# Performance work log

Measured on AMD Instinct MI355X. Metric: run time of the kernel, lower is better.

## Reference

```python
import jax, jax.numpy as jnp
import numpy as np

N_NODES = 100000
N_EDGES = 1600000
D = 64


def setup_inputs() -> dict:
    key = jax.random.key(0)
    k0, k1, k2, k3 = jax.random.split(key, 4)
    x = jax.random.normal(k0, (N_NODES, D), dtype=jnp.float32)
    edge_index = jax.random.randint(k1, (2, N_EDGES), 0, N_NODES, dtype=jnp.int64)
    W1 = jax.random.normal(k2, (D, D), dtype=jnp.float32) * 0.1
    b1 = jnp.zeros((D,), dtype=jnp.float32)
    W2 = jax.random.normal(k3, (D, D), dtype=jnp.float32) * 0.1
    b2 = jnp.zeros((D,), dtype=jnp.float32)
    return {"x": x, "edge_index": edge_index, "W1": W1, "b1": b1, "W2": W2, "b2": b2}


def _gcn_layer(x, edge_index, W, b):
    n = x.shape[0]
    h = x @ W  # [N, Dout] -- transform before aggregation (small GEMM)
    loop = jnp.arange(n, dtype=edge_index.dtype)
    src = jnp.concatenate([edge_index[0], loop])
    dst = jnp.concatenate([edge_index[1], loop])
    deg = jax.ops.segment_sum(jnp.ones_like(dst, dtype=h.dtype), dst, num_segments=n)
    dinv = jax.lax.rsqrt(deg)  # deg >= 1 thanks to self loops
    norm = dinv[src] * dinv[dst]  # [E+N]
    msg = h[src] * norm[:, None]  # gather: [E+N, Dout]
    agg = jax.ops.segment_sum(msg, dst, num_segments=n)  # scatter-add
    return agg + b


def reference(x, edge_index, W1, b1, W2, b2):
    # dropout p = 0.0 -> identity
    h = jax.nn.relu(_gcn_layer(x, edge_index, W1, b1))
    h = jax.nn.relu(_gcn_layer(h, edge_index, W2, b2))
    return h
```

## Files before the change

kernel.cpp:

```cpp
#include <hip/hip_runtime.h>
#include <hip/hip_bf16.h>

#define D 64
#define NB_HIST 256
#define MAXBK 512

typedef float vfloat4 __attribute__((ext_vector_type(4)));

__device__ __forceinline__ unsigned short f2bf(float f) {
    union { float f; unsigned u; } v; v.f = f;
    unsigned r = (v.u + 0x7FFF + ((v.u >> 16) & 1)) >> 16;
    return (unsigned short)r;
}
__device__ __forceinline__ float bflo(unsigned u) {
    union { unsigned u; float f; } v; v.u = u << 16; return v.f;
}
__device__ __forceinline__ float bfhi(unsigned u) {
    union { unsigned u; float f; } v; v.u = u & 0xFFFF0000u; return v.f;
}

__global__ __launch_bounds__(256) void passA_gemm(
    const int* __restrict__ dst, int* __restrict__ blockCounts, int E, int per, int NBK,
    const float* __restrict__ X, const float* __restrict__ W,
    unsigned short* __restrict__ hn, int N)
{
    int tid = threadIdx.x;

    if ((int)blockIdx.x < NB_HIST) {
        __shared__ int hist[MAXBK];
        for (int i = tid; i < NBK; i += 256) hist[i] = 0;
        __syncthreads();
        int lo = blockIdx.x * per, hi = min(E, lo + per);
        for (int i = lo + tid * 4; i < hi; i += 1024) {
            if (i + 3 < hi) {
                int4 d4 = *(const int4*)(dst + i);
                atomicAdd(&hist[d4.x >> 8], 1);
                atomicAdd(&hist[d4.y >> 8], 1);
                atomicAdd(&hist[d4.z >> 8], 1);
                atomicAdd(&hist[d4.w >> 8], 1);
            } else {
                for (int k = i; k < hi; ++k) atomicAdd(&hist[dst[k] >> 8], 1);
            }
        }
        __syncthreads();
        for (int i = tid; i < NBK; i += 256)
            blockCounts[(size_t)blockIdx.x * NBK + i] = hist[i];
        return;
    }

    __shared__ float sW[D * D];
    __shared__ float sX[32 * D];
    int rowBase = ((int)blockIdx.x - NB_HIST) * 32;

    for (int i = tid; i < 1024; i += 256)
        ((vfloat4*)sW)[i] = ((const vfloat4*)W)[i];
    for (int i = tid; i < 512; i += 256) {
        int r = rowBase + (i >> 4);
        vfloat4 v = (vfloat4)0.0f;
        if (r < N) v = __builtin_nontemporal_load(((const vfloat4*)X) + rowBase * 16 + i);
        ((vfloat4*)sX)[i] = v;
    }
    __syncthreads();

    int wave = tid >> 6, lane = tid & 63;
    float accv[8];
#pragma unroll
    for (int r = 0; r < 8; ++r) accv[r] = 0.0f;
    int xoff = (wave * 8) * D;
#pragma unroll 8
    for (int k = 0; k < D; ++k) {
        float wv = sW[k * D + lane];
#pragma unroll
        for (int r = 0; r < 8; ++r)
            accv[r] += sX[xoff + r * D + k] * wv;
    }
#pragma unroll
    for (int r = 0; r < 8; ++r) {
        int row = rowBase + wave * 8 + r;
        if (row < N) hn[(size_t)row * D + lane] = f2bf(accv[r]);
    }
}

__global__ __launch_bounds__(256) void scan_cols(
    const int* __restrict__ blockCounts, int* __restrict__ partial,
    int* __restrict__ totals, int NBK)
{
    int wave = threadIdx.x >> 6, lane = threadIdx.x & 63;
    int k = blockIdx.x * 4 + wave;
    if (k >= NBK) return;
    int carry = 0;
    for (int base = 0; base < NB_HIST; base += 64) {
        int b = base + lane;
        int v = blockCounts[(size_t)b * NBK + k];
        int inc = v;
        for (int d = 1; d < 64; d <<= 1) {
            int t = __shfl_up(inc, d, 64);
            if (lane >= d) inc += t;
        }
        partial[(size_t)k * NB_HIST + b] = inc - v + carry;
        carry += __shfl(inc, 63, 64);
    }
    if (lane == 0) totals[k] = carry;
}

__global__ void scan_buckets(const int* __restrict__ totals, int* __restrict__ bofs, int NBK) {
    int lane = threadIdx.x;
    int carry = 0;
    for (int base = 0; base < NBK; base += 64) {
        int i = base + lane;
        int v = (i < NBK) ? totals[i] : 0;
        int inc = v;
        for (int d = 1; d < 64; d <<= 1) {
            int t = __shfl_up(inc, d, 64);
            if (lane >= d) inc += t;
        }
        if (i < NBK) bofs[i] = inc - v + carry;
        carry += __shfl(inc, 63, 64);
    }
}

__global__ __launch_bounds__(256) void passB(
    const int* __restrict__ src, const int* __restrict__ dst,
    const int* __restrict__ bofs, const int* __restrict__ partial,
    int* __restrict__ bucketed, int E, int per, int NBK)
{
    __shared__ int cur[MAXBK];
    int tid = threadIdx.x, b = blockIdx.x;
    for (int i = tid; i < NBK; i += 256)
        cur[i] = bofs[i] + partial[(size_t)i * NB_HIST + b];
    __syncthreads();
    int lo = b * per, hi = min(E, lo + per);
    for (int i = lo + tid * 4; i < hi; i += 1024) {
        if (i + 3 < hi) {
            int4 d4 = *(const int4*)(dst + i);
            int4 s4 = *(const int4*)(src + i);
            int p0 = atomicAdd(&cur[d4.x >> 8], 1);
            int p1 = atomicAdd(&cur[d4.y >> 8], 1);
            int p2 = atomicAdd(&cur[d4.z >> 8], 1);
            int p3 = atomicAdd(&cur[d4.w >> 8], 1);
            bucketed[p0] = (s4.x << 8) | (d4.x & 255);
            bucketed[p1] = (s4.y << 8) | (d4.y & 255);
            bucketed[p2] = (s4.z << 8) | (d4.z & 255);
            bucketed[p3] = (s4.w << 8) | (d4.w & 255);
        } else {
            for (int k = i; k < hi; ++k) {
                int d = dst[k], s = src[k];
                int pos = atomicAdd(&cur[d >> 8], 1);
                bucketed[pos] = (s << 8) | (d & 255);
            }
        }
    }
}

__global__ __launch_bounds__(256) void build_csr_scale(
    const int* __restrict__ bucketed, const int* __restrict__ bofs,
    const int* __restrict__ totals, int* __restrict__ deg, float* __restrict__ dinv,
    int* __restrict__ ofs, int* __restrict__ csr,
    unsigned short* __restrict__ hn, int N)
{
    __shared__ int h[256];
    __shared__ int scn[256];
    __shared__ float sdv[256];
    int tid = threadIdx.x, k = blockIdx.x;
    int e0 = bofs[k], e1 = e0 + totals[k];
    int node = k * 256 + tid;

    h[tid] = 0;
    __syncthreads();
    for (int i = e0 + tid; i < e1; i += 256)
        atomicAdd(&h[bucketed[i] & 255], 1);
    __syncthreads();

    int mydeg = h[tid];
    scn[tid] = mydeg;
    __syncthreads();
    for (int d2 = 1; d2 < 256; d2 <<= 1) {
        int t = (tid >= d2) ? scn[tid - d2] : 0;
        __syncthreads();
        scn[tid] += t;
        __syncthreads();
    }
    int myofs = scn[tid] - mydeg;

    float dv = rsqrtf((float)(mydeg + 1));
    sdv[tid] = dv;
    if (node < N) {
        deg[node]  = mydeg;
        dinv[node] = dv;
        ofs[node]  = e0 + myofs;
    }

    h[tid] = myofs;
    __syncthreads();
    for (int i = e0 + tid; i < e1; i += 256) {
        int v = bucketed[i];
        int pos = atomicAdd(&h[v & 255], 1);
        csr[e0 + pos] = v >> 8;
    }

    __syncthreads();
    int4* hp = (int4*)hn;
    for (int c = tid; c < 2048; c += 256) {
        int r = c >> 3;
        int n2 = k * 256 + r;
        if (n2 < N) {
            float f = sdv[r];
            size_t idx = (size_t)n2 * 8 + (c & 7);
            int4 hv = hp[idx];
            unsigned r0 = (unsigned)f2bf(bflo(hv.x) * f) | ((unsigned)f2bf(bfhi(hv.x) * f) << 16);
            unsigned r1 = (unsigned)f2bf(bflo(hv.y) * f) | ((unsigned)f2bf(bfhi(hv.y) * f) << 16);
            unsigned r2 = (unsigned)f2bf(bflo(hv.z) * f) | ((unsigned)f2bf(bfhi(hv.z) * f) << 16);
            unsigned r3 = (unsigned)f2bf(bflo(hv.w) * f) | ((unsigned)f2bf(bfhi(hv.w) * f) << 16);
            hp[idx] = make_int4((int)r0, (int)r1, (int)r2, (int)r3);
        }
    }
}

__global__ __launch_bounds__(256) void gemm2(
    const float* __restrict__ X, const float* __restrict__ W,
    const float* __restrict__ dinv, unsigned short* __restrict__ hn, int N)
{
    __shared__ float sW[D * D];
    __shared__ float sX[32 * D];
    int tid = threadIdx.x;
    int rowBase = blockIdx.x * 32;

    for (int i = tid; i < 1024; i += 256)
        ((vfloat4*)sW)[i] = ((const vfloat4*)W)[i];
    for (int i = tid; i < 512; i += 256) {
        int r = rowBase + (i >> 4);
        vfloat4 v = (vfloat4)0.0f;
        if (r < N) v = ((const vfloat4*)X)[rowBase * 16 + i];
        ((vfloat4*)sX)[i] = v;
    }
    __syncthreads();

    int wave = tid >> 6, lane = tid & 63;
    float accv[8];
#pragma unroll
    for (int r = 0; r < 8; ++r) accv[r] = 0.0f;
    int xoff = (wave * 8) * D;
#pragma unroll 8
    for (int k = 0; k < D; ++k) {
        float wv = sW[k * D + lane];
#pragma unroll
        for (int r = 0; r < 8; ++r)
            accv[r] += sX[xoff + r * D + k] * wv;
    }
#pragma unroll
    for (int r = 0; r < 8; ++r) {
        int row = rowBase + wave * 8 + r;
        if (row < N) hn[(size_t)row * D + lane] = f2bf(accv[r] * dinv[row]);
    }
}

__global__ __launch_bounds__(256) void aggregate_relu(
    const int* __restrict__ ofs, const int* __restrict__ deg,
    const int* __restrict__ csr, const unsigned short* __restrict__ hn,
    const float* __restrict__ dinv, const float* __restrict__ bias,
    float* __restrict__ out, int N)
{
    int t    = blockIdx.x * 256 + threadIdx.x;
    int lane = threadIdx.x & 63;
    int grp  = lane >> 3, sub = lane & 7;
    int node = (t >> 6) * 8 + grp;
    bool live = (node < N);

    const int4* hrow = (const int4*)hn;
    float2 a0 = {0.f, 0.f}, a1 = {0.f, 0.f}, a2 = {0.f, 0.f}, a3 = {0.f, 0.f};

    int s0 = 0, cnt = 0;
    if (live) {
        s0  = ofs[node];
        cnt = deg[node];
        int4 h = hrow[(size_t)node * 8 + sub];
        a0.x += bflo(h.x); a0.y += bfhi(h.x);
        a1.x += bflo(h.y); a1.y += bfhi(h.y);
        a2.x += bflo(h.z); a2.y += bfhi(h.z);
        a3.x += bflo(h.w); a3.y += bfhi(h.w);
    }

    const int* cp = csr + s0;
    int j = 0;
    for (; j + 1 < cnt; j += 2) {
        int sA = cp[j], sB = cp[j + 1];
        int4 hA = hrow[(size_t)sA * 8 + sub];
        int4 hB = hrow[(size_t)sB * 8 + sub];
        a0.x += bflo(hA.x); a0.y += bfhi(hA.x);
        a1.x += bflo(hA.y); a1.y += bfhi(hA.y);
        a2.x += bflo(hA.z); a2.y += bfhi(hA.z);
        a3.x += bflo(hA.w); a3.y += bfhi(hA.w);
        a0.x += bflo(hB.x); a0.y += bfhi(hB.x);
        a1.x += bflo(hB.y); a1.y += bfhi(hB.y);
        a2.x += bflo(hB.z); a2.y += bfhi(hB.z);
        a3.x += bflo(hB.w); a3.y += bfhi(hB.w);
    }
    if (j < cnt) {
        int sA = cp[j];
        int4 hA = hrow[(size_t)sA * 8 + sub];
        a0.x += bflo(hA.x); a0.y += bfhi(hA.x);
        a1.x += bflo(hA.y); a1.y += bfhi(hA.y);
        a2.x += bflo(hA.z); a2.y += bfhi(hA.z);
        a3.x += bflo(hA.w); a3.y += bfhi(hA.w);
    }

    if (live) {
        float dw = dinv[node];
        float4 b0 = ((const float4*)bias)[sub * 2];
        float4 b1 = ((const float4*)bias)[sub * 2 + 1];
        float4 o0, o1;
        o0.x = fmaxf(a0.x * dw + b0.x, 0.f);
        o0.y = fmaxf(a0.y * dw + b0.y, 0.f);
        o0.z = fmaxf(a1.x * dw + b0.z, 0.f);
        o0.w = fmaxf(a1.y * dw + b0.w, 0.f);
        o1.x = fmaxf(a2.x * dw + b1.x, 0.f);
        o1.y = fmaxf(a2.y * dw + b1.y, 0.f);
        o1.z = fmaxf(a3.x * dw + b1.z, 0.f);
        o1.w = fmaxf(a3.y * dw + b1.w, 0.f);
        ((float4*)out)[(size_t)node * 16 + sub * 2]     = o0;
        ((float4*)out)[(size_t)node * 16 + sub * 2 + 1] = o1;
    }
}


extern "C" void kernel_launch(void* const* d_in, const int* in_sizes, int n_in,
                              void* d_out, int out_size, void* d_ws, size_t ws_size,
                              hipStream_t stream) {
    const float* x   = (const float*)d_in[0];
    const int*   ei  = (const int*)d_in[1];
    const float* b1  = (const float*)d_in[3];
    const float* W1  = (const float*)d_in[2];
    const float* W2  = (const float*)d_in[4];
    const float* b2  = (const float*)d_in[5];

    int N = in_sizes[0] / D;
    int E = in_sizes[1] / 2;
    const int* src = ei;
    const int* dst = ei + E;
    int NBK = (N + 255) >> 8;
    int per = (((E + NB_HIST - 1) / NB_HIST) + 3) & ~3;

    char* ws = (char*)d_ws;
    int*            blockCounts = (int*)(ws + 0x00000000);
    int*            partial     = (int*)(ws + 0x00080000);
    int*            totals      = (int*)(ws + 0x00100000);
    int*            bofs        = (int*)(ws + 0x00110000);
    int*            deg         = (int*)(ws + 0x00120000);
    float*          dinv        = (float*)(ws + 0x00190000);
    int*            ofs         = (int*)(ws + 0x00200000);
    int*            bucketed    = (int*)(ws + 0x00280000);
    int*            csr         = (int*)(ws + 0x00A00000);
    unsigned short* hn          = (unsigned short*)(ws + 0x01100000);
    float*          outF        = (float*)d_out;

    int nb_G = (N + 31) / 32;
    int nb_A = (N + 31) / 32;

    passA_gemm<<<NB_HIST + nb_G, 256, 0, stream>>>(dst, blockCounts, E, per, NBK, x, W1, hn, N);
    scan_cols<<<(NBK + 3) / 4, 256, 0, stream>>>(blockCounts, partial, totals, NBK);
    scan_buckets<<<1, 64, 0, stream>>>(totals, bofs, NBK);
    passB<<<NB_HIST, 256, 0, stream>>>(src, dst, bofs, partial, bucketed, E, per, NBK);
    build_csr_scale<<<NBK, 256, 0, stream>>>(bucketed, bofs, totals, deg, dinv, ofs, csr, hn, N);

    aggregate_relu<<<nb_A, 256, 0, stream>>>(ofs, deg, csr, hn, dinv, b1, outF, N);
    gemm2<<<nb_G, 256, 0, stream>>>(outF, W2, dinv, hn, N);
    aggregate_relu<<<nb_A, 256, 0, stream>>>(ofs, deg, csr, hn, dinv, b2, outF, N);
}
```

Baseline: 242.8 us.

## Split bf16 feature table into four column slices for cache-local gathers

Stores the bf16 transformed features as four slices of 16 columns each, laid out contiguously per slice, and has each aggregation block handle only one slice for 128 nodes. The intent is to shrink the working set for each random gather pass so the slice fits better in L2/MALL, cutting cache misses when fetching neighbor rows. In exchange, each gather now touches only 32 bytes per neighbor, and the CSR indices are read four times, once per slice, so there are more launches' worth of blocks and more index traffic.

```diff
diff --git a/kernel.cpp b/kernel.cpp
--- a/kernel.cpp
+++ b/kernel.cpp
@@ -18,6 +18,7 @@
 __device__ __forceinline__ float bfhi(unsigned u) {
     union { unsigned u; float f; } v; v.u = u & 0xFFFF0000u; return v.f;
 }
+
 
 __global__ __launch_bounds__(256) void passA_gemm(
     const int* __restrict__ dst, int* __restrict__ blockCounts, int E, int per, int NBK,
@@ -74,10 +75,12 @@
         for (int r = 0; r < 8; ++r)
             accv[r] += sX[xoff + r * D + k] * wv;
     }
+    size_t sbase = (size_t)(lane >> 4) * ((size_t)N * 16);
+    int within = lane & 15;
 #pragma unroll
     for (int r = 0; r < 8; ++r) {
         int row = rowBase + wave * 8 + r;
-        if (row < N) hn[(size_t)row * D + lane] = f2bf(accv[r]);
+        if (row < N) hn[sbase + (size_t)row * 16 + within] = f2bf(accv[r]);
     }
 }
 
@@ -200,12 +203,15 @@
 
     __syncthreads();
     int4* hp = (int4*)hn;
+    size_t sstride = (size_t)N * 2;
     for (int c = tid; c < 2048; c += 256) {
-        int r = c >> 3;
+        int slice = c >> 9;
+        int r = (c >> 1) & 255;
+        int half = c & 1;
         int n2 = k * 256 + r;
         if (n2 < N) {
             float f = sdv[r];
-            size_t idx = (size_t)n2 * 8 + (c & 7);
+            size_t idx = (size_t)slice * sstride + (size_t)n2 * 2 + half;
             int4 hv = hp[idx];
             unsigned r0 = (unsigned)f2bf(bflo(hv.x) * f) | ((unsigned)f2bf(bfhi(hv.x) * f) << 16);
             unsigned r1 = (unsigned)f2bf(bflo(hv.y) * f) | ((unsigned)f2bf(bfhi(hv.y) * f) << 16);
@@ -247,10 +253,12 @@
         for (int r = 0; r < 8; ++r)
             accv[r] += sX[xoff + r * D + k] * wv;
     }
+    size_t sbase = (size_t)(lane >> 4) * ((size_t)N * 16);
+    int within = lane & 15;
 #pragma unroll
     for (int r = 0; r < 8; ++r) {
         int row = rowBase + wave * 8 + r;
-        if (row < N) hn[(size_t)row * D + lane] = f2bf(accv[r] * dinv[row]);
+        if (row < N) hn[sbase + (size_t)row * 16 + within] = f2bf(accv[r] * dinv[row]);
     }
 }
 
@@ -260,20 +268,21 @@
     const float* __restrict__ dinv, const float* __restrict__ bias,
     float* __restrict__ out, int N)
 {
-    int t    = blockIdx.x * 256 + threadIdx.x;
-    int lane = threadIdx.x & 63;
-    int grp  = lane >> 3, sub = lane & 7;
-    int node = (t >> 6) * 8 + grp;
+    int slice = blockIdx.x & 3;
+    int tblk  = blockIdx.x >> 2;
+    int tid   = threadIdx.x;
+    int pair  = tid >> 1, half = tid & 1;
+    int node  = tblk * 128 + pair;
     bool live = (node < N);
 
-    const int4* hrow = (const int4*)hn;
+    const int4* base = (const int4*)hn + (size_t)slice * ((size_t)N * 2);
     float2 a0 = {0.f, 0.f}, a1 = {0.f, 0.f}, a2 = {0.f, 0.f}, a3 = {0.f, 0.f};
 
     int s0 = 0, cnt = 0;
     if (live) {
         s0  = ofs[node];
         cnt = deg[node];
-        int4 h = hrow[(size_t)node * 8 + sub];
+        int4 h = base[(size_t)node * 2 + half];
         a0.x += bflo(h.x); a0.y += bfhi(h.x);
         a1.x += bflo(h.y); a1.y += bfhi(h.y);
         a2.x += bflo(h.z); a2.y += bfhi(h.z);
@@ -284,8 +293,8 @@
     int j = 0;
     for (; j + 1 < cnt; j += 2) {
         int sA = cp[j], sB = cp[j + 1];
-        int4 hA = hrow[(size_t)sA * 8 + sub];
-        int4 hB = hrow[(size_t)sB * 8 + sub];
+        int4 hA = base[(size_t)sA * 2 + half];
+        int4 hB = base[(size_t)sB * 2 + half];
         a0.x += bflo(hA.x); a0.y += bfhi(hA.x);
         a1.x += bflo(hA.y); a1.y += bfhi(hA.y);
         a2.x += bflo(hA.z); a2.y += bfhi(hA.z);
@@ -297,7 +306,7 @@
     }
     if (j < cnt) {
         int sA = cp[j];
-        int4 hA = hrow[(size_t)sA * 8 + sub];
+        int4 hA = base[(size_t)sA * 2 + half];
         a0.x += bflo(hA.x); a0.y += bfhi(hA.x);
         a1.x += bflo(hA.y); a1.y += bfhi(hA.y);
         a2.x += bflo(hA.z); a2.y += bfhi(hA.z);
@@ -306,8 +315,8 @@
 
     if (live) {
         float dw = dinv[node];
-        float4 b0 = ((const float4*)bias)[sub * 2];
-        float4 b1 = ((const float4*)bias)[sub * 2 + 1];
+        float4 b0 = ((const float4*)bias)[slice * 4 + half * 2];
+        float4 b1 = ((const float4*)bias)[slice * 4 + half * 2 + 1];
         float4 o0, o1;
         o0.x = fmaxf(a0.x * dw + b0.x, 0.f);
         o0.y = fmaxf(a0.y * dw + b0.y, 0.f);
@@ -317,8 +326,8 @@
         o1.y = fmaxf(a2.y * dw + b1.y, 0.f);
         o1.z = fmaxf(a3.x * dw + b1.z, 0.f);
         o1.w = fmaxf(a3.y * dw + b1.w, 0.f);
-        ((float4*)out)[(size_t)node * 16 + sub * 2]     = o0;
-        ((float4*)out)[(size_t)node * 16 + sub * 2 + 1] = o1;
+        ((float4*)out)[(size_t)node * 16 + slice * 4 + half * 2]     = o0;
+        ((float4*)out)[(size_t)node * 16 + slice * 4 + half * 2 + 1] = o1;
     }
 }
 
@@ -328,8 +337,8 @@
                               hipStream_t stream) {
     const float* x   = (const float*)d_in[0];
     const int*   ei  = (const int*)d_in[1];
+    const float* W1  = (const float*)d_in[2];
     const float* b1  = (const float*)d_in[3];
-    const float* W1  = (const float*)d_in[2];
     const float* W2  = (const float*)d_in[4];
     const float* b2  = (const float*)d_in[5];
 
@@ -354,7 +363,7 @@
     float*          outF        = (float*)d_out;
 
     int nb_G = (N + 31) / 32;
-    int nb_A = (N + 31) / 32;
+    int nb_A = ((N + 127) / 128) * 4;
 
     passA_gemm<<<NB_HIST + nb_G, 256, 0, stream>>>(dst, blockCounts, E, per, NBK, x, W1, hn, N);
     scan_cols<<<(NBK + 3) / 4, 256, 0, stream>>>(blockCounts, partial, totals, NBK);
```

Measured after the change: 288.1 us. 1.19x slower.
